# Kernel optimization log

Measured on AMD Instinct MI355X. Metric: run time of the kernel, lower is better.

The kernel has to match this reference:

```python
import jax, jax.numpy as jnp
import numpy as np

WIN = 10  # self.len in the torch module


def setup_inputs() -> dict:
    key = jax.random.key(0)
    # [batch, seq_length, agent_num, vel]
    inputs = jax.random.normal(key, (8, 512, 96, 2), dtype=jnp.float32)
    return {"inputs": inputs}


def reference(inputs):
    # Faithful vectorization of the triple loop:
    #                    / sqrt(sum xc_i^2 * sum xc_j^2)
    # (the (seq_length*vel - 1) normalizers in cov/std cancel exactly)
    B, S, A, V = inputs.shape
    xc = inputs - inputs.mean(axis=1, keepdims=True)  # center over time
    # per-timestep pairwise Gram over the tiny vel dim: [B, S, A, A]
    g = jnp.einsum('bsiv,bsjv->bsij', xc, xc)
    # sliding-window sums via cumulative-sum trick
    C = jnp.cumsum(g, axis=1)                         # [B, S, A, A]
    head = C[:, :S - 1]                               # window end at step s (s=1..S-1)
    tail = jnp.concatenate(
        [jnp.zeros((B, WIN, A, A), C.dtype), C[:, :S - 1 - WIN]], axis=1)
    W = head - tail                                   # windowed Gram [B, S-1, A, A]
    d = jnp.diagonal(W, axis1=2, axis2=3)             # windowed energy [B, S-1, A]
    corr = W / jnp.sqrt(d[..., :, None] * d[..., None, :])
    # torch code never writes the diagonal -> stays zero
    mask = 1.0 - jnp.eye(A, dtype=corr.dtype)
    return corr * mask
```

## Files before the change

kernel.cpp:

```cpp
#include <hip/hip_runtime.h>

constexpr int WIN = 10;
constexpr int Bn  = 8;
constexpr int Sn  = 512;
constexpr int An  = 96;
constexpr int Tn  = Sn - 1;
constexpr int AV  = An * 2;

constexpr int SCHUNK = 32;
constexpr int NCH    = Sn / SCHUNK;
constexpr int CH     = 8;
constexpr int CHUNKS_PER_B = (Tn + CH - 1) / CH;
constexpr int MAXROWS = CH + WIN - 1;
constexpr int ISPLIT  = 2;
constexpr int RPT     = (An / ISPLIT) / 8;

__global__ __launch_bounds__(192)
void partial_kernel(const float* __restrict__ in, float* __restrict__ partial) {
    const int blk = blockIdx.x;
    const int b   = blk / NCH;
    const int c   = blk - b * NCH;
    const int av  = threadIdx.x;
    const float* p = in + ((size_t)(b * Sn + c * SCHUNK)) * AV + av;
    float acc = 0.f;
    #pragma unroll
    for (int s = 0; s < SCHUNK; ++s) acc += p[(size_t)s * AV];
    partial[(size_t)blk * AV + av] = acc;
}

__global__ __launch_bounds__(256)
void reduce_kernel(const float* __restrict__ partial, float* __restrict__ sums) {
    int idx = blockIdx.x * blockDim.x + threadIdx.x;
    if (idx >= Bn * AV) return;
    int b  = idx / AV;
    int av = idx - b * AV;
    float acc = 0.f;
    #pragma unroll
    for (int c = 0; c < NCH; ++c) acc += partial[(size_t)(b * NCH + c) * AV + av];
    sums[idx] = acc;
}

__global__ __launch_bounds__(256)
void corr_kernel(const float* __restrict__ in, const float* __restrict__ sums,
                 float* __restrict__ out) {
    __shared__ float xw[MAXROWS * AV];

    const int bid   = blockIdx.x;
    const int b     = bid / (CHUNKS_PER_B * ISPLIT);
    const int rem   = bid - b * (CHUNKS_PER_B * ISPLIT);
    const int chunk = rem >> 1;
    const int half  = rem & 1;
    const int i0    = half * (An / ISPLIT);

    const int t0 = chunk * CH;
    const int t1 = min(t0 + CH - 1, Tn - 1);
    int sbase = t0 - (WIN - 1); if (sbase < 0) sbase = 0;
    const int nrows = t1 - sbase + 1;

    const int tid = threadIdx.x;

    {
        const float4* src = reinterpret_cast<const float4*>(
            in + ((size_t)(b * Sn + sbase)) * AV);
        const float4* mb = reinterpret_cast<const float4*>(sums + b * AV);
        float4* dst = reinterpret_cast<float4*>(xw);
        const int tot4 = nrows * (AV / 4);
        constexpr float invS = 1.0f / Sn;
        for (int idx = tid; idx < tot4; idx += 256) {
            int av4 = idx % (AV / 4);
            float4 v = src[idx], m = mb[av4];
            v.x -= m.x * invS; v.y -= m.y * invS;
            v.z -= m.z * invS; v.w -= m.w * invS;
            dst[idx] = v;
        }
    }
    __syncthreads();

    const int tx = tid & 31;
    const int ty = tid >> 5;

    float acc[RPT][3];
    float di[RPT], dj[3];
    #pragma unroll
    for (int r = 0; r < RPT; ++r) {
        di[r] = 0.f;
        #pragma unroll
        for (int c = 0; c < 3; ++c) acc[r][c] = 0.f;
    }
    #pragma unroll
    for (int c = 0; c < 3; ++c) dj[c] = 0.f;

#define ACCUM(ls, OP)                                                       \
    {                                                                       \
        const float* xs = &xw[(ls) * AV];                                   \
        float2 xj[3];                                                       \
        _Pragma("unroll")                                                   \
        for (int c = 0; c < 3; ++c) {                                       \
            xj[c] = *reinterpret_cast<const float2*>(&xs[(tx + 32 * c) * 2]);\
            dj[c] OP (xj[c].x * xj[c].x + xj[c].y * xj[c].y);               \
        }                                                                   \
        _Pragma("unroll")                                                   \
        for (int r = 0; r < RPT; ++r) {                                     \
            float2 xi = *reinterpret_cast<const float2*>(                   \
                &xs[(i0 + ty + 8 * r) * 2]);                                \
            di[r] OP (xi.x * xi.x + xi.y * xi.y);                           \
            _Pragma("unroll")                                               \
            for (int c = 0; c < 3; ++c)                                     \
                acc[r][c] OP (xi.x * xj[c].x + xi.y * xj[c].y);             \
        }                                                                   \
    }

    auto emit = [&](int t) {
        float rsj[3];
        #pragma unroll
        for (int c = 0; c < 3; ++c) rsj[c] = rsqrtf(dj[c]);
        float* ob = out + (size_t)(b * Tn + t) * (An * An);
        #pragma unroll
        for (int r = 0; r < RPT; ++r) {
            int i = i0 + ty + 8 * r;
            float ri = rsqrtf(di[r]);
            #pragma unroll
            for (int c = 0; c < 3; ++c) {
                int j = tx + 32 * c;
                float v = (i == j) ? 0.f : acc[r][c] * ri * rsj[c];
                ob[(size_t)i * An + j] = v;
            }
        }
    };

    for (int s = sbase; s <= t0; ++s) ACCUM(s - sbase, +=);
    emit(t0);

    for (int t = t0 + 1; t <= t1; ++t) {
        ACCUM(t - sbase, +=);
        if (t >= WIN) ACCUM(t - WIN - sbase, -=);
        emit(t);
    }
#undef ACCUM
}

extern "C" void kernel_launch(void* const* d_in, const int* in_sizes, int n_in,
                              void* d_out, int out_size, void* d_ws, size_t ws_size,
                              hipStream_t stream) {
    const float* in = (const float*)d_in[0];
    float* out = (float*)d_out;
    float* sums    = (float*)d_ws;
    float* partial = (float*)d_ws + Bn * AV;

    partial_kernel<<<Bn * NCH, 192, 0, stream>>>(in, partial);
    reduce_kernel<<<(Bn * AV + 255) / 256, 256, 0, stream>>>(partial, sums);
    corr_kernel<<<Bn * CHUNKS_PER_B * ISPLIT, 256, 0, stream>>>(in, sums, out);
}
```

Before: 40.92 us.

## Fuse mean reduction into corr kernel and vectorize output stores with float4

Drops the separate reduce kernel: each corr block now sums the per-chunk partials itself into shared memory, which removes one launch and its global round trip. The thread mapping changes to 192 threads with 24 columns by 8 rows, so each thread owns 4 contiguous output columns and writes them as one float4 store. Time chunks grow from 8 to 16 steps and rows are split into quarters. The cost is redundant partial-sum reads in every block and a different occupancy profile.

Measured after the change: 40.58 us. About the same (-0.8%).

```diff
diff --git a/kernel.cpp b/kernel.cpp
--- a/kernel.cpp
+++ b/kernel.cpp
@@ -9,11 +9,15 @@
 
 constexpr int SCHUNK = 32;
 constexpr int NCH    = Sn / SCHUNK;
-constexpr int CH     = 8;
+constexpr int CH     = 16;
 constexpr int CHUNKS_PER_B = (Tn + CH - 1) / CH;
 constexpr int MAXROWS = CH + WIN - 1;
-constexpr int ISPLIT  = 2;
-constexpr int RPT     = (An / ISPLIT) / 8;
+constexpr int ISPLIT  = 4;
+constexpr int ROWS    = An / ISPLIT;
+constexpr int NTHR    = 192;
+constexpr int TXN     = 24;
+constexpr int TYN     = NTHR / TXN;
+constexpr int RPT     = ROWS / TYN;
 
 __global__ __launch_bounds__(192)
 void partial_kernel(const float* __restrict__ in, float* __restrict__ partial) {
@@ -28,29 +32,18 @@
     partial[(size_t)blk * AV + av] = acc;
 }
 
-__global__ __launch_bounds__(256)
-void reduce_kernel(const float* __restrict__ partial, float* __restrict__ sums) {
-    int idx = blockIdx.x * blockDim.x + threadIdx.x;
-    if (idx >= Bn * AV) return;
-    int b  = idx / AV;
-    int av = idx - b * AV;
-    float acc = 0.f;
-    #pragma unroll
-    for (int c = 0; c < NCH; ++c) acc += partial[(size_t)(b * NCH + c) * AV + av];
-    sums[idx] = acc;
-}
+__global__ __launch_bounds__(192)
+void corr_kernel(const float* __restrict__ in, const float* __restrict__ partial,
+                 float* __restrict__ out) {
+    __shared__ __align__(16) float xw[MAXROWS * AV];
+    __shared__ __align__(16) float smu[AV];
 
-__global__ __launch_bounds__(256)
-void corr_kernel(const float* __restrict__ in, const float* __restrict__ sums,
-                 float* __restrict__ out) {
-    __shared__ float xw[MAXROWS * AV];
-
-    const int bid   = blockIdx.x;
-    const int b     = bid / (CHUNKS_PER_B * ISPLIT);
-    const int rem   = bid - b * (CHUNKS_PER_B * ISPLIT);
-    const int chunk = rem >> 1;
-    const int half  = rem & 1;
-    const int i0    = half * (An / ISPLIT);
+    const int bid     = blockIdx.x;
+    const int b       = bid / (CHUNKS_PER_B * ISPLIT);
+    const int rem     = bid - b * (CHUNKS_PER_B * ISPLIT);
+    const int chunk   = rem >> 2;
+    const int quarter = rem & 3;
+    const int i0      = quarter * ROWS;
 
     const int t0 = chunk * CH;
     const int t1 = min(t0 + CH - 1, Tn - 1);
@@ -60,71 +53,79 @@
     const int tid = threadIdx.x;
 
     {
+        const float* pp = partial + (size_t)b * NCH * AV + tid;
+        float acc = 0.f;
+        #pragma unroll
+        for (int c = 0; c < NCH; ++c) acc += pp[(size_t)c * AV];
+        smu[tid] = acc * (1.0f / Sn);
+    }
+    __syncthreads();
+
+    {
         const float4* src = reinterpret_cast<const float4*>(
             in + ((size_t)(b * Sn + sbase)) * AV);
-        const float4* mb = reinterpret_cast<const float4*>(sums + b * AV);
+        const float4* mb4 = reinterpret_cast<const float4*>(smu);
         float4* dst = reinterpret_cast<float4*>(xw);
         const int tot4 = nrows * (AV / 4);
-        constexpr float invS = 1.0f / Sn;
-        for (int idx = tid; idx < tot4; idx += 256) {
+        for (int idx = tid; idx < tot4; idx += NTHR) {
             int av4 = idx % (AV / 4);
-            float4 v = src[idx], m = mb[av4];
-            v.x -= m.x * invS; v.y -= m.y * invS;
-            v.z -= m.z * invS; v.w -= m.w * invS;
+            float4 v = src[idx], m = mb4[av4];
+            v.x -= m.x; v.y -= m.y; v.z -= m.z; v.w -= m.w;
             dst[idx] = v;
         }
     }
     __syncthreads();
 
-    const int tx = tid & 31;
-    const int ty = tid >> 5;
+    const int tx = tid % TXN;
+    const int ty = tid / TXN;
 
-    float acc[RPT][3];
-    float di[RPT], dj[3];
+    float acc[RPT][4];
+    float di[RPT], dj[4];
     #pragma unroll
     for (int r = 0; r < RPT; ++r) {
         di[r] = 0.f;
         #pragma unroll
-        for (int c = 0; c < 3; ++c) acc[r][c] = 0.f;
+        for (int c = 0; c < 4; ++c) acc[r][c] = 0.f;
     }
     #pragma unroll
-    for (int c = 0; c < 3; ++c) dj[c] = 0.f;
+    for (int c = 0; c < 4; ++c) dj[c] = 0.f;
 
-#define ACCUM(ls, OP)                                                       \
-    {                                                                       \
-        const float* xs = &xw[(ls) * AV];                                   \
-        float2 xj[3];                                                       \
-        _Pragma("unroll")                                                   \
-        for (int c = 0; c < 3; ++c) {                                       \
-            xj[c] = *reinterpret_cast<const float2*>(&xs[(tx + 32 * c) * 2]);\
-            dj[c] OP (xj[c].x * xj[c].x + xj[c].y * xj[c].y);               \
-        }                                                                   \
-        _Pragma("unroll")                                                   \
-        for (int r = 0; r < RPT; ++r) {                                     \
-            float2 xi = *reinterpret_cast<const float2*>(                   \
-                &xs[(i0 + ty + 8 * r) * 2]);                                \
-            di[r] OP (xi.x * xi.x + xi.y * xi.y);                           \
-            _Pragma("unroll")                                               \
-            for (int c = 0; c < 3; ++c)                                     \
-                acc[r][c] OP (xi.x * xj[c].x + xi.y * xj[c].y);             \
-        }                                                                   \
+#define ACCUM(ls, OP)                                                        \
+    {                                                                        \
+        const float* xs = &xw[(ls) * AV];                                    \
+        float4 xj0 = *reinterpret_cast<const float4*>(&xs[8 * tx]);          \
+        float4 xj1 = *reinterpret_cast<const float4*>(&xs[8 * tx + 4]);      \
+        dj[0] OP (xj0.x * xj0.x + xj0.y * xj0.y);                            \
+        dj[1] OP (xj0.z * xj0.z + xj0.w * xj0.w);                            \
+        dj[2] OP (xj1.x * xj1.x + xj1.y * xj1.y);                            \
+        dj[3] OP (xj1.z * xj1.z + xj1.w * xj1.w);                            \
+        _Pragma("unroll")                                                    \
+        for (int r = 0; r < RPT; ++r) {                                      \
+            float2 xi = *reinterpret_cast<const float2*>(                    \
+                &xs[(i0 + ty + 8 * r) * 2]);                                 \
+            di[r] OP (xi.x * xi.x + xi.y * xi.y);                            \
+            acc[r][0] OP (xi.x * xj0.x + xi.y * xj0.y);                      \
+            acc[r][1] OP (xi.x * xj0.z + xi.y * xj0.w);                      \
+            acc[r][2] OP (xi.x * xj1.x + xi.y * xj1.y);                      \
+            acc[r][3] OP (xi.x * xj1.z + xi.y * xj1.w);                      \
+        }                                                                    \
     }
 
     auto emit = [&](int t) {
-        float rsj[3];
+        float rsj[4];
         #pragma unroll
-        for (int c = 0; c < 3; ++c) rsj[c] = rsqrtf(dj[c]);
+        for (int c = 0; c < 4; ++c) rsj[c] = rsqrtf(dj[c]);
         float* ob = out + (size_t)(b * Tn + t) * (An * An);
         #pragma unroll
         for (int r = 0; r < RPT; ++r) {
             int i = i0 + ty + 8 * r;
             float ri = rsqrtf(di[r]);
-            #pragma unroll
-            for (int c = 0; c < 3; ++c) {
-                int j = tx + 32 * c;
-                float v = (i == j) ? 0.f : acc[r][c] * ri * rsj[c];
-                ob[(size_t)i * An + j] = v;
-            }
+            float4 v;
+            v.x = (i == 4 * tx + 0) ? 0.f : acc[r][0] * ri * rsj[0];
+            v.y = (i == 4 * tx + 1) ? 0.f : acc[r][1] * ri * rsj[1];
+            v.z = (i == 4 * tx + 2) ? 0.f : acc[r][2] * ri * rsj[2];
+            v.w = (i == 4 * tx + 3) ? 0.f : acc[r][3] * ri * rsj[3];
+            *reinterpret_cast<float4*>(&ob[(size_t)i * An + 4 * tx]) = v;
         }
     };
 
@@ -144,10 +145,8 @@
                               hipStream_t stream) {
     const float* in = (const float*)d_in[0];
     float* out = (float*)d_out;
-    float* sums    = (float*)d_ws;
-    float* partial = (float*)d_ws + Bn * AV;
+    float* partial = (float*)d_ws;
 
     partial_kernel<<<Bn * NCH, 192, 0, stream>>>(in, partial);
-    reduce_kernel<<<(Bn * AV + 255) / 256, 256, 0, stream>>>(partial, sums);
-    corr_kernel<<<Bn * CHUNKS_PER_B * ISPLIT, 256, 0, stream>>>(in, sums, out);
+    corr_kernel<<<Bn * CHUNKS_PER_B * ISPLIT, NTHR, 0, stream>>>(in, partial, out);
 }
```
